# Kernel tuning notes

Hardware: AMD Instinct MI355X
Metric: run time of the kernel (lower is better)

The kernel has to match this reference:

```python
import jax, jax.numpy as jnp
import numpy as np

B, S, D, H = 4, 2048, 1024, 16
HD = D // H  # head_dim = 64

def setup_inputs() -> dict:
    key = jax.random.key(0)
    ks = jax.random.split(key, 5)
    scale = 1.0 / np.sqrt(D)
    return {
        "x": jax.random.normal(ks[0], (B, S, D), dtype=jnp.float32),
        "Wqkv": jax.random.normal(ks[1], (D, 3 * D), dtype=jnp.float32) * scale,
        "bqkv": jax.random.normal(ks[2], (3 * D,), dtype=jnp.float32) * 0.01,
        "Wo": jax.random.normal(ks[3], (D, D), dtype=jnp.float32) * scale,
        "bo": jax.random.normal(ks[4], (D,), dtype=jnp.float32) * 0.01,
    }

def reference(x, Wqkv, bqkv, Wo, bo):
    b, s, d = x.shape
    # fused QKV projection: [B,S,3D]
    qkv = jnp.einsum("bsd,de->bse", x, Wqkv) + bqkv
    # [B,S,H,3*HD] -> [B,H,S,3*HD], then chunk into q,k,v per head
    qkv = qkv.reshape(b, s, H, 3 * HD).transpose(0, 2, 1, 3)
    q, k, v = jnp.split(qkv, 3, axis=-1)  # each [B,H,S,HD]
    inv_sqrt_dk = jnp.asarray(1.0 / np.sqrt(HD), dtype=x.dtype)
    scores = jnp.einsum("bhqd,bhkd->bhqk", q, k) * inv_sqrt_dk
    attn = jax.nn.softmax(scores, axis=-1)
    values = jnp.einsum("bhqk,bhkd->bhqd", attn, v)  # [B,H,S,HD]
    # NOTE: source reshapes [B,H,S,HD] -> [B,S,H*HD] WITHOUT permuting back
    # (a quirk of the original code); replicated faithfully.
    values = values.reshape(b, s, d)
    out = jnp.einsum("bsd,de->bse", values, Wo) + bo
    return out
```

## Files before the change

kernel.cpp:

```cpp
#include <hip/hip_runtime.h>
#include <hip/hip_bf16.h>
#include <cstdint>

static constexpr int Bq  = 4;
static constexpr int Sq  = 2048;
static constexpr int Dq  = 1024;
static constexpr int Hq  = 16;
static constexpr int HDq = 64;
static constexpr int ROWS = Bq * Sq;
static constexpr int QKV_N = 3 * Dq;

typedef __bf16 bf16x8 __attribute__((ext_vector_type(8)));
typedef __bf16 bf16x4 __attribute__((ext_vector_type(4)));
typedef __bf16 bf16x2 __attribute__((ext_vector_type(2)));
typedef float  floatx4 __attribute__((ext_vector_type(4)));
typedef float  floatx16 __attribute__((ext_vector_type(16)));
typedef unsigned int uintx4 __attribute__((ext_vector_type(4)));

#define MFMA16(a, b, c) __builtin_amdgcn_mfma_f32_16x16x32_bf16((a), (b), (c), 0, 0, 0)
#define MFMA32(a, b, c) __builtin_amdgcn_mfma_f32_32x32x16_bf16((a), (b), (c), 0, 0, 0)

#define QSCALE 0.18033688011112042f

__device__ __forceinline__ void async16(const void* g, void* l) {
    __builtin_amdgcn_global_load_lds(
        (const __attribute__((address_space(1))) uint32_t*)g,
        (__attribute__((address_space(3))) uint32_t*)l, 16, 0, 0);
}

__global__ __launch_bounds__(256) void prep_kernel(const float4* __restrict__ x4,
                                                   bf16x4* __restrict__ xb4,
                                                   const float* __restrict__ Wqkv,
                                                   __bf16* __restrict__ WqkvT,
                                                   const float* __restrict__ Wo,
                                                   __bf16* __restrict__ WoT) {
    __shared__ float t[32][33];
    const int bx = blockIdx.x;
    if (bx < 8192) {
        int i = bx * 256 + threadIdx.x;
        float4 v = x4[i];
        bf16x4 o;
        o[0] = (__bf16)v.x; o[1] = (__bf16)v.y; o[2] = (__bf16)v.z; o[3] = (__bf16)v.w;
        xb4[i] = o;
        return;
    }
    const float* in; __bf16* out; int K, N, bid;
    if (bx < 8192 + 3072) { bid = bx - 8192;  in = Wqkv; out = WqkvT; K = Dq; N = QKV_N; }
    else                  { bid = bx - 11264; in = Wo;   out = WoT;   K = Dq; N = Dq; }
    const int nt = N / 32;
    const int n0 = (bid % nt) * 32, k0 = (bid / nt) * 32;
    const int c = threadIdx.x & 31, r0 = threadIdx.x >> 5;
#pragma unroll
    for (int rr = 0; rr < 32; rr += 8)
        t[r0 + rr][c] = in[(size_t)(k0 + r0 + rr) * N + n0 + c];
    __syncthreads();
#pragma unroll
    for (int rr = 0; rr < 32; rr += 8)
        out[(size_t)(n0 + r0 + rr) * K + k0 + c] = (__bf16)t[c][r0 + rr];
}

__global__ __launch_bounds__(512, 2) void gemm_qkv_kernel(const __bf16* __restrict__ A,
                                                          const __bf16* __restrict__ BT,
                                                          const float* __restrict__ bias,
                                                          __bf16* __restrict__ qkvb,
                                                          __bf16* __restrict__ Vt) {
    __shared__ __bf16 lds[2][2][2][128][64];

    const int tid  = threadIdx.x;
    const int lane = tid & 63;
    const int wave = tid >> 6;
    const int wm = wave >> 2;
    const int wn = wave & 3;
    const int l31 = lane & 31;
    const int hi  = lane >> 5;
    const int kx  = l31 & 7;

    const int m0 = blockIdx.y * 256;
    const int n0 = blockIdx.x * 256;

    const int srow = lane >> 3;
    const int ssl  = ((lane & 7) ^ srow) * 8;
    const __bf16* gA = A  + (size_t)(m0 + wave * 16 + srow) * 1024 + ssl;
    const __bf16* gB = BT + (size_t)(n0 + wave * 16 + srow) * 1024 + ssl;

    auto STAGE = [&](int buf, int op, int half, int ktel) {
        const __bf16* g = (op ? gB : gA) + (size_t)half * (128 * 1024) + ktel;
        __bf16* l = &lds[buf][op][half][0][0] + wave * 1024 + lane * 8;
        async16(g, l);
        async16(g + 8 * 1024, l + 512);
    };

    floatx16 acc[4][2] = {};

    STAGE(0, 1, 0, 0);
    STAGE(0, 0, 0, 0);
    STAGE(0, 1, 1, 0);
    STAGE(0, 0, 1, 0);
    STAGE(1, 1, 0, 64);
    STAGE(1, 0, 0, 64);
    asm volatile("s_waitcnt vmcnt(4)" ::: "memory");
    __builtin_amdgcn_sched_barrier(0);
    __builtin_amdgcn_s_barrier();

    const int brow = (wn & 1) * 64;

    for (int t = 0; t < 16; ++t) {
        const int d = t & 1;
        const __bf16* As = &lds[d][0][wm][0][0];
        const __bf16* Bs = &lds[d][1][wn >> 1][0][0];

        bf16x8 af[2][4], bf0[4], bf1[4];

#pragma unroll
        for (int mf = 0; mf < 2; ++mf)
#pragma unroll
            for (int ks = 0; ks < 4; ++ks)
                af[mf][ks] = *(const bf16x8*)(As + (mf * 32 + l31) * 64 + ((ks * 2 + hi) ^ kx) * 8);
#pragma unroll
        for (int ks = 0; ks < 4; ++ks)
            bf0[ks] = *(const bf16x8*)(Bs + (brow + l31) * 64 + ((ks * 2 + hi) ^ kx) * 8);
        if (t + 1 < 16) STAGE(d ^ 1, 1, 1, (t + 1) * 64);
        __builtin_amdgcn_s_barrier();
        __builtin_amdgcn_s_setprio(1);
#pragma unroll
        for (int ks = 0; ks < 4; ++ks) {
            acc[0][0] = MFMA32(af[0][ks], bf0[ks], acc[0][0]);
            acc[1][0] = MFMA32(af[1][ks], bf0[ks], acc[1][0]);
        }
        __builtin_amdgcn_s_setprio(0);
        __builtin_amdgcn_s_barrier();

#pragma unroll
        for (int ks = 0; ks < 4; ++ks)
            bf1[ks] = *(const bf16x8*)(Bs + (brow + 32 + l31) * 64 + ((ks * 2 + hi) ^ kx) * 8);
        if (t + 1 < 16) STAGE(d ^ 1, 0, 1, (t + 1) * 64);
        __builtin_amdgcn_s_barrier();
        __builtin_amdgcn_s_setprio(1);
#pragma unroll
        for (int ks = 0; ks < 4; ++ks) {
            acc[0][1] = MFMA32(af[0][ks], bf1[ks], acc[0][1]);
            acc[1][1] = MFMA32(af[1][ks], bf1[ks], acc[1][1]);
        }
        __builtin_amdgcn_s_setprio(0);
        __builtin_amdgcn_s_barrier();

#pragma unroll
        for (int mf = 0; mf < 2; ++mf)
#pragma unroll
            for (int ks = 0; ks < 4; ++ks)
                af[mf][ks] = *(const bf16x8*)(As + ((2 + mf) * 32 + l31) * 64 + ((ks * 2 + hi) ^ kx) * 8);
        if (t + 2 < 16) STAGE(d, 1, 0, (t + 2) * 64);
        __builtin_amdgcn_s_barrier();
        __builtin_amdgcn_s_setprio(1);
#pragma unroll
        for (int ks = 0; ks < 4; ++ks) {
            acc[2][1] = MFMA32(af[0][ks], bf1[ks], acc[2][1]);
            acc[3][1] = MFMA32(af[1][ks], bf1[ks], acc[3][1]);
        }
        __builtin_amdgcn_s_setprio(0);
        __builtin_amdgcn_s_barrier();

        if (t + 2 < 16) STAGE(d, 0, 0, (t + 2) * 64);
        __builtin_amdgcn_s_barrier();
        __builtin_amdgcn_s_setprio(1);
#pragma unroll
        for (int ks = 0; ks < 4; ++ks) {
            acc[2][0] = MFMA32(af[0][ks], bf0[ks], acc[2][0]);
            acc[3][0] = MFMA32(af[1][ks], bf0[ks], acc[3][0]);
        }
        __builtin_amdgcn_s_setprio(0);
        if (t < 14) {
            asm volatile("s_waitcnt vmcnt(4)" ::: "memory");
        } else {
            asm volatile("s_waitcnt vmcnt(0)" ::: "memory");
        }
        __builtin_amdgcn_sched_barrier(0);
        __builtin_amdgcn_s_barrier();
    }

#pragma unroll
    for (int fn = 0; fn < 2; ++fn) {
        const int cg = n0 + wn * 64 + fn * 32;
        const int cm = cg % 192;
        const float bv = bias[cg + l31];
        if (cm >= 128) {
            const int hh = cg / 192;
            const int dd = cm - 128 + l31;
            const int bb = m0 >> 11;
            const int sb = (m0 + wm * 128) & 2047;
            __bf16* vt = Vt + ((size_t)(bb * Hq + hh) * HDq + dd) * Sq + sb;
#pragma unroll
            for (int fm = 0; fm < 4; ++fm)
#pragma unroll
                for (int g = 0; g < 4; ++g) {
                    bf16x4 vv;
#pragma unroll
                    for (int i = 0; i < 4; ++i) vv[i] = (__bf16)(acc[fm][fn][g * 4 + i] + bv);
                    *(bf16x4*)(vt + fm * 32 + g * 8 + hi * 4) = vv;
                }
        } else {
            const float sc = (cm < 64) ? QSCALE : 1.0f;
#pragma unroll
            for (int fm = 0; fm < 4; ++fm)
#pragma unroll
                for (int r = 0; r < 16; ++r) {
                    int m = m0 + wm * 128 + fm * 32 + (r & 3) + 8 * (r >> 2) + 4 * hi;
                    qkvb[(size_t)m * QKV_N + cg + l31] = (__bf16)((acc[fm][fn][r] + bv) * sc);
                }
        }
    }
}

__global__ __launch_bounds__(256) void gemm_out_kernel(const __bf16* __restrict__ A,
                                                       const __bf16* __restrict__ BT,
                                                       const float* __restrict__ bias,
                                                       float* __restrict__ Cout,
                                                       int M, int N, int K) {
    __shared__ __bf16 As[128 * 32];
    __shared__ __bf16 Bs[128 * 32];

    const int t = threadIdx.x;
    const int lane = t & 63;
    const int wave = t >> 6;
    const int wm = wave & 1, wn = wave >> 1;
    const int l15 = lane & 15;
    const int kg = (lane >> 4) * 8;

    const int m0 = blockIdx.y * 128;
    const int n0 = blockIdx.x * 128;

    const int srow = t >> 2;
    const int scol = (t & 3) * 8;
    const __bf16* ag = A  + (size_t)(m0 + srow) * K + scol;
    const __bf16* bg = BT + (size_t)(n0 + srow) * K + scol;
    __bf16* al = As + t * 8;
    __bf16* bl = Bs + t * 8;

    floatx4 acc[4][4] = {};

    for (int k0 = 0; k0 < K; k0 += 32) {
        __syncthreads();
        async16(ag + k0,                    al);
        async16(ag + (size_t)64 * K + k0,   al + 2048);
        async16(bg + k0,                    bl);
        async16(bg + (size_t)64 * K + k0,   bl + 2048);
        __syncthreads();

        bf16x8 af[4], bfr[4];
#pragma unroll
        for (int mi = 0; mi < 4; ++mi)
            af[mi] = *(const bf16x8*)(As + (wm * 64 + mi * 16 + l15) * 32 + kg);
#pragma unroll
        for (int ni = 0; ni < 4; ++ni)
            bfr[ni] = *(const bf16x8*)(Bs + (wn * 64 + ni * 16 + l15) * 32 + kg);
#pragma unroll
        for (int mi = 0; mi < 4; ++mi)
#pragma unroll
            for (int ni = 0; ni < 4; ++ni)
                acc[mi][ni] = MFMA16(af[mi], bfr[ni], acc[mi][ni]);
    }

    const int r0 = (lane >> 4) * 4;
    const int wn0 = n0 + wn * 64;

#pragma unroll
    for (int ni = 0; ni < 4; ++ni) {
        int col = wn0 + ni * 16 + l15;
        float bv = bias[col];
#pragma unroll
        for (int mi = 0; mi < 4; ++mi) {
#pragma unroll
            for (int i = 0; i < 4; ++i) {
                int row = m0 + wm * 64 + mi * 16 + r0 + i;
                Cout[(size_t)row * N + col] = acc[mi][ni][i] + bv;
            }
        }
    }
}

__global__ __launch_bounds__(256, 2) void attn_kernel(const __bf16* __restrict__ qkv,
                                                      const __bf16* __restrict__ Vt,
                                                      __bf16* __restrict__ v2) {
    const int bh = blockIdx.x;
    const int b = bh >> 4, h = bh & 15;
    const int q0 = blockIdx.y * 256;
    const int tid  = threadIdx.x;
    const int lane = tid & 63;
    const int wave = tid >> 6;
    const int l31  = lane & 31;
    const int hi   = lane >> 5;
    const int kx   = l31 & 7;
    const size_t rs = QKV_N;
    const __bf16* base  = qkv + (size_t)b * Sq * rs + (size_t)h * (3 * HDq);
    const __bf16* vbase = Vt + (size_t)bh * HDq * Sq;

    __shared__ alignas(16) __bf16 Ks[2][64][64];
    __shared__ alignas(16) __bf16 Vs[2][64][64];

    bf16x8 qb[2][4];
#pragma unroll
    for (int qg = 0; qg < 2; ++qg) {
        const __bf16* qr = base + (size_t)(q0 + wave * 64 + qg * 32 + l31) * rs + hi * 8;
#pragma unroll
        for (int st = 0; st < 4; ++st) qb[qg][st] = *(const bf16x8*)(qr + st * 16);
    }

    const int rA = wave * 8 + (lane >> 3);
    const int rB = rA + 32;
    const int sw = ((lane & 7) ^ (rA & 7)) * 8;
    const __bf16* gK0 = base + HDq + (size_t)rA * rs + sw;
    const __bf16* gK1 = base + HDq + (size_t)rB * rs + sw;
    const __bf16* gV0 = vbase + (size_t)rA * Sq + sw;
    const __bf16* gV1 = vbase + (size_t)rB * Sq + sw;
    const int loff0 = wave * 512 + lane * 8;
    const int loff1 = (4 + wave) * 512 + lane * 8;

    auto STAGE = [&](int bufi, int kt) {
        const size_t ko = (size_t)kt * rs;
        async16(gK0 + ko, &Ks[bufi][0][0] + loff0);
        async16(gK1 + ko, &Ks[bufi][0][0] + loff1);
        async16(gV0 + kt, &Vs[bufi][0][0] + loff0);
        async16(gV1 + kt, &Vs[bufi][0][0] + loff1);
    };

    auto softmax_pb = [&](const floatx16& c, float& la, bf16x8* pb) {
        unsigned int W[8];
        float s0 = 0.f, s1 = 0.f;
#pragma unroll
        for (int m = 0; m < 8; ++m) {
            float e0 = __builtin_amdgcn_exp2f(c[2 * m]);
            float e1 = __builtin_amdgcn_exp2f(c[2 * m + 1]);
            s0 += e0; s1 += e1;
            union { bf16x2 v; unsigned int u; } pk;
            pk.v[0] = (__bf16)e0; pk.v[1] = (__bf16)e1;
            W[m] = pk.u;
        }
        la += s0 + s1;
#pragma unroll
        for (int ks = 0; ks < 2; ++ks) {
            auto r0 = __builtin_amdgcn_permlane32_swap(W[ks * 4 + 0], W[ks * 4 + 2], false, false);
            auto r1 = __builtin_amdgcn_permlane32_swap(W[ks * 4 + 1], W[ks * 4 + 3], false, false);
            uintx4 bb; bb[0] = r0[0]; bb[1] = r1[0]; bb[2] = r0[1]; bb[3] = r1[1];
            pb[ks] = __builtin_bit_cast(bf16x8, bb);
        }
    };

    floatx16 o[2][2] = {};
    float la0 = 0.f, la1 = 0.f;

    STAGE(0, 0);
    __syncthreads();

    int cur = 0;
    for (int kt = 0; kt < Sq; kt += 64, cur ^= 1) {
        if (kt + 64 < Sq) STAGE(cur ^ 1, kt + 64);

        bf16x8 ka0[4], ka1[4];
#pragma unroll
        for (int st = 0; st < 4; ++st) {
            ka0[st] = *(const bf16x8*)(&Ks[cur][l31][((st * 2 + hi) ^ kx) * 8]);
            ka1[st] = *(const bf16x8*)(&Ks[cur][32 + l31][((st * 2 + hi) ^ kx) * 8]);
        }
        floatx16 c00 = {}, c01 = {}, c10 = {}, c11 = {};
        __builtin_amdgcn_s_setprio(1);
#pragma unroll
        for (int st = 0; st < 4; ++st) {
            c00 = MFMA32(ka0[st], qb[0][st], c00);
            c10 = MFMA32(ka1[st], qb[0][st], c10);
            c01 = MFMA32(ka0[st], qb[1][st], c01);
            c11 = MFMA32(ka1[st], qb[1][st], c11);
        }
        __builtin_amdgcn_s_setprio(0);

        bf16x8 pb00[2], pb01[2], pb10[2], pb11[2];
        softmax_pb(c00, la0, pb00);
        softmax_pb(c01, la1, pb01);
        __builtin_amdgcn_s_setprio(1);
#pragma unroll
        for (int ks = 0; ks < 2; ++ks) {
            const int kslot = ks * 2 + hi;
            bf16x8 va0 = *(const bf16x8*)(&Vs[cur][l31][(kslot ^ kx) * 8]);
            bf16x8 va1 = *(const bf16x8*)(&Vs[cur][32 + l31][(kslot ^ kx) * 8]);
            o[0][0] = MFMA32(va0, pb00[ks], o[0][0]);
            o[0][1] = MFMA32(va1, pb00[ks], o[0][1]);
            o[1][0] = MFMA32(va0, pb01[ks], o[1][0]);
            o[1][1] = MFMA32(va1, pb01[ks], o[1][1]);
        }
        __builtin_amdgcn_s_setprio(0);
        softmax_pb(c10, la0, pb10);
        softmax_pb(c11, la1, pb11);
        __builtin_amdgcn_s_setprio(1);
#pragma unroll
        for (int ks = 0; ks < 2; ++ks) {
            const int kslot = 4 + ks * 2 + hi;
            bf16x8 va0 = *(const bf16x8*)(&Vs[cur][l31][(kslot ^ kx) * 8]);
            bf16x8 va1 = *(const bf16x8*)(&Vs[cur][32 + l31][(kslot ^ kx) * 8]);
            o[0][0] = MFMA32(va0, pb10[ks], o[0][0]);
            o[0][1] = MFMA32(va1, pb10[ks], o[0][1]);
            o[1][0] = MFMA32(va0, pb11[ks], o[1][0]);
            o[1][1] = MFMA32(va1, pb11[ks], o[1][1]);
        }
        __builtin_amdgcn_s_setprio(0);

        __syncthreads();
    }

#pragma unroll
    for (int qg = 0; qg < 2; ++qg) {
        float lsum = qg ? la1 : la0;
        float l = lsum + __shfl_xor(lsum, 32);
        float rinv = 1.0f / l;
        const int q = q0 + wave * 64 + qg * 32 + l31;
        size_t row = (size_t)b * Sq + h * 128 + (q >> 4);
        __bf16* vrow = v2 + row * Dq + (size_t)(q & 15) * 64;
#pragma unroll
        for (int gg = 0; gg < 4; ++gg) {
            bf16x4 ov;
#pragma unroll
            for (int i = 0; i < 4; ++i) ov[i] = (__bf16)(o[qg][0][gg * 4 + i] * rinv);
            *(bf16x4*)(vrow + gg * 8 + hi * 4) = ov;
#pragma unroll
            for (int i = 0; i < 4; ++i) ov[i] = (__bf16)(o[qg][1][gg * 4 + i] * rinv);
            *(bf16x4*)(vrow + 32 + gg * 8 + hi * 4) = ov;
        }
    }
}

extern "C" void kernel_launch(void* const* d_in, const int* in_sizes, int n_in,
                              void* d_out, int out_size, void* d_ws, size_t ws_size,
                              hipStream_t stream) {
    const float* x    = (const float*)d_in[0];
    const float* Wqkv = (const float*)d_in[1];
    const float* bqkv = (const float*)d_in[2];
    const float* Wo   = (const float*)d_in[3];
    const float* bo   = (const float*)d_in[4];
    float* out = (float*)d_out;

    __bf16* xb    = (__bf16*)d_ws;
    __bf16* WqkvT = xb    + (size_t)ROWS * Dq;
    __bf16* WoT   = WqkvT + (size_t)QKV_N * Dq;
    __bf16* qkvb  = WoT   + (size_t)Dq * Dq;
    __bf16* Vt    = qkvb  + (size_t)ROWS * QKV_N;
    __bf16* v2    = xb;

    prep_kernel<<<12288, 256, 0, stream>>>((const float4*)x, (bf16x4*)xb,
                                           Wqkv, WqkvT, Wo, WoT);

    gemm_qkv_kernel<<<dim3(QKV_N / 256, ROWS / 256), 512, 0, stream>>>(
        xb, WqkvT, bqkv, qkvb, Vt);

    attn_kernel<<<dim3(Bq * Hq, Sq / 256), 256, 0, stream>>>(qkvb, Vt, v2);

    gemm_out_kernel<<<dim3(Dq / 128, ROWS / 128), 256, 0, stream>>>(
        v2, WoT, bo, out, ROWS, Dq, Dq);
}
```

Before: 269.6 us.

## Retile QKV GEMM to 256x192 head-aligned blocks with 4x2 wave layout

```diff
diff --git a/kernel.cpp b/kernel.cpp
--- a/kernel.cpp
+++ b/kernel.cpp
@@ -64,109 +64,110 @@
                                                           const float* __restrict__ bias,
                                                           __bf16* __restrict__ qkvb,
                                                           __bf16* __restrict__ Vt) {
-    __shared__ __bf16 lds[2][2][2][128][64];
+    __shared__ __bf16 lds[2][7][64][64];
 
     const int tid  = threadIdx.x;
     const int lane = tid & 63;
     const int wave = tid >> 6;
-    const int wm = wave >> 2;
-    const int wn = wave & 3;
+    const int wm = wave >> 1;
+    const int wn = wave & 1;
     const int l31 = lane & 31;
     const int hi  = lane >> 5;
     const int kx  = l31 & 7;
 
     const int m0 = blockIdx.y * 256;
-    const int n0 = blockIdx.x * 256;
-
-    const int srow = lane >> 3;
-    const int ssl  = ((lane & 7) ^ srow) * 8;
-    const __bf16* gA = A  + (size_t)(m0 + wave * 16 + srow) * 1024 + ssl;
-    const __bf16* gB = BT + (size_t)(n0 + wave * 16 + srow) * 1024 + ssl;
-
-    auto STAGE = [&](int buf, int op, int half, int ktel) {
-        const __bf16* g = (op ? gB : gA) + (size_t)half * (128 * 1024) + ktel;
-        __bf16* l = &lds[buf][op][half][0][0] + wave * 1024 + lane * 8;
-        async16(g, l);
-        async16(g + 8 * 1024, l + 512);
+    const int n0 = blockIdx.x * 192;
+
+    const int sw = ((lane & 7) ^ (lane >> 3)) * 8;
+    const __bf16* gA = A  + (size_t)(m0 + wave * 8 + (lane >> 3)) * 1024 + sw;
+    const __bf16* gB = BT + (size_t)(n0 + wave * 8 + (lane >> 3)) * 1024 + sw;
+
+    auto STAGEA = [&](int buf, int u, int ktel) {
+        async16(gA + (size_t)u * 65536 + ktel, &lds[buf][u][0][0] + wave * 512 + lane * 8);
     };
-
-    floatx16 acc[4][2] = {};
-
-    STAGE(0, 1, 0, 0);
-    STAGE(0, 0, 0, 0);
-    STAGE(0, 1, 1, 0);
-    STAGE(0, 0, 1, 0);
-    STAGE(1, 1, 0, 64);
-    STAGE(1, 0, 0, 64);
+    auto STAGEB = [&](int buf, int j, int ktel) {
+        async16(gB + (size_t)j * 65536 + ktel, &lds[buf][4 + j][0][0] + wave * 512 + lane * 8);
+    };
+
+    floatx16 acc[2][3] = {};
+
+#pragma unroll
+    for (int u = 0; u < 4; ++u) STAGEA(0, u, 0);
+#pragma unroll
+    for (int j = 0; j < 3; ++j) STAGEB(0, j, 0);
+#pragma unroll
+    for (int u = 0; u < 4; ++u) STAGEA(1, u, 64);
     asm volatile("s_waitcnt vmcnt(4)" ::: "memory");
     __builtin_amdgcn_sched_barrier(0);
     __builtin_amdgcn_s_barrier();
 
-    const int brow = (wn & 1) * 64;
+    bf16x8 af[2][4], bf[4];
 
     for (int t = 0; t < 16; ++t) {
         const int d = t & 1;
-        const __bf16* As = &lds[d][0][wm][0][0];
-        const __bf16* Bs = &lds[d][1][wn >> 1][0][0];
-
-        bf16x8 af[2][4], bf0[4], bf1[4];
-
-#pragma unroll
-        for (int mf = 0; mf < 2; ++mf)
+
+#pragma unroll
+        for (int fm = 0; fm < 2; ++fm)
 #pragma unroll
             for (int ks = 0; ks < 4; ++ks)
-                af[mf][ks] = *(const bf16x8*)(As + (mf * 32 + l31) * 64 + ((ks * 2 + hi) ^ kx) * 8);
-#pragma unroll
-        for (int ks = 0; ks < 4; ++ks)
-            bf0[ks] = *(const bf16x8*)(Bs + (brow + l31) * 64 + ((ks * 2 + hi) ^ kx) * 8);
-        if (t + 1 < 16) STAGE(d ^ 1, 1, 1, (t + 1) * 64);
+                af[fm][ks] = *(const bf16x8*)(&lds[d][wm][fm * 32 + l31][((ks * 2 + hi) ^ kx) * 8]);
+        {
+            const int br = wn * 96;
+#pragma unroll
+            for (int ks = 0; ks < 4; ++ks)
+                bf[ks] = *(const bf16x8*)(&lds[d][4 + (br >> 6)][(br & 63) + l31][((ks * 2 + hi) ^ kx) * 8]);
+        }
+        if (t + 1 < 16) {
+            STAGEB(d ^ 1, 0, (t + 1) * 64);
+            STAGEB(d ^ 1, 1, (t + 1) * 64);
+            STAGEB(d ^ 1, 2, (t + 1) * 64);
+        }
         __builtin_amdgcn_s_barrier();
         __builtin_amdgcn_s_setprio(1);
 #pragma unroll
         for (int ks = 0; ks < 4; ++ks) {
-            acc[0][0] = MFMA32(af[0][ks], bf0[ks], acc[0][0]);
-            acc[1][0] = MFMA32(af[1][ks], bf0[ks], acc[1][0]);
-        }
-        __builtin_amdgcn_s_setprio(0);
-        __builtin_amdgcn_s_barrier();
-
-#pragma unroll
-        for (int ks = 0; ks < 4; ++ks)
-            bf1[ks] = *(const bf16x8*)(Bs + (brow + 32 + l31) * 64 + ((ks * 2 + hi) ^ kx) * 8);
-        if (t + 1 < 16) STAGE(d ^ 1, 0, 1, (t + 1) * 64);
+            acc[0][0] = MFMA32(af[0][ks], bf[ks], acc[0][0]);
+            acc[1][0] = MFMA32(af[1][ks], bf[ks], acc[1][0]);
+        }
+        __builtin_amdgcn_s_setprio(0);
+        __builtin_amdgcn_s_barrier();
+
+        {
+            const int br = wn * 96 + 32;
+#pragma unroll
+            for (int ks = 0; ks < 4; ++ks)
+                bf[ks] = *(const bf16x8*)(&lds[d][4 + (br >> 6)][(br & 63) + l31][((ks * 2 + hi) ^ kx) * 8]);
+        }
+        if (t + 2 < 16) {
+            STAGEA(d, 0, (t + 2) * 64);
+            STAGEA(d, 1, (t + 2) * 64);
+        }
         __builtin_amdgcn_s_barrier();
         __builtin_amdgcn_s_setprio(1);
 #pragma unroll
         for (int ks = 0; ks < 4; ++ks) {
-            acc[0][1] = MFMA32(af[0][ks], bf1[ks], acc[0][1]);
-            acc[1][1] = MFMA32(af[1][ks], bf1[ks], acc[1][1]);
-        }
-        __builtin_amdgcn_s_setprio(0);
-        __builtin_amdgcn_s_barrier();
-
-#pragma unroll
-        for (int mf = 0; mf < 2; ++mf)
+            acc[0][1] = MFMA32(af[0][ks], bf[ks], acc[0][1]);
+            acc[1][1] = MFMA32(af[1][ks], bf[ks], acc[1][1]);
+        }
+        __builtin_amdgcn_s_setprio(0);
+        __builtin_amdgcn_s_barrier();
+
+        {
+            const int br = wn * 96 + 64;
 #pragma unroll
             for (int ks = 0; ks < 4; ++ks)
-                af[mf][ks] = *(const bf16x8*)(As + ((2 + mf) * 32 + l31) * 64 + ((ks * 2 + hi) ^ kx) * 8);
-        if (t + 2 < 16) STAGE(d, 1, 0, (t + 2) * 64);
+                bf[ks] = *(const bf16x8*)(&lds[d][4 + (br >> 6)][(br & 63) + l31][((ks * 2 + hi) ^ kx) * 8]);
+        }
+        if (t + 2 < 16) {
+            STAGEA(d, 2, (t + 2) * 64);
+            STAGEA(d, 3, (t + 2) * 64);
+        }
         __builtin_amdgcn_s_barrier();
         __builtin_amdgcn_s_setprio(1);
 #pragma unroll
         for (int ks = 0; ks < 4; ++ks) {
-            acc[2][1] = MFMA32(af[0][ks], bf1[ks], acc[2][1]);
-            acc[3][1] = MFMA32(af[1][ks], bf1[ks], acc[3][1]);
-        }
-        __builtin_amdgcn_s_setprio(0);
-        __builtin_amdgcn_s_barrier();
-
-        if (t + 2 < 16) STAGE(d, 0, 0, (t + 2) * 64);
-        __builtin_amdgcn_s_barrier();
-        __builtin_amdgcn_s_setprio(1);
-#pragma unroll
-        for (int ks = 0; ks < 4; ++ks) {
-            acc[2][0] = MFMA32(af[0][ks], bf0[ks], acc[2][0]);
-            acc[3][0] = MFMA32(af[1][ks], bf0[ks], acc[3][0]);
+            acc[0][2] = MFMA32(af[0][ks], bf[ks], acc[0][2]);
+            acc[1][2] = MFMA32(af[1][ks], bf[ks], acc[1][2]);
         }
         __builtin_amdgcn_s_setprio(0);
         if (t < 14) {
@@ -179,18 +180,18 @@
     }
 
 #pragma unroll
-    for (int fn = 0; fn < 2; ++fn) {
-        const int cg = n0 + wn * 64 + fn * 32;
-        const int cm = cg % 192;
+    for (int fn = 0; fn < 3; ++fn) {
+        const int cm = wn * 96 + fn * 32;
+        const int cg = n0 + cm;
         const float bv = bias[cg + l31];
         if (cm >= 128) {
-            const int hh = cg / 192;
+            const int hh = n0 / 192;
             const int dd = cm - 128 + l31;
             const int bb = m0 >> 11;
-            const int sb = (m0 + wm * 128) & 2047;
+            const int sb = (m0 & 2047) + wm * 64;
             __bf16* vt = Vt + ((size_t)(bb * Hq + hh) * HDq + dd) * Sq + sb;
 #pragma unroll
-            for (int fm = 0; fm < 4; ++fm)
+            for (int fm = 0; fm < 2; ++fm)
 #pragma unroll
                 for (int g = 0; g < 4; ++g) {
                     bf16x4 vv;
@@ -201,10 +202,10 @@
         } else {
             const float sc = (cm < 64) ? QSCALE : 1.0f;
 #pragma unroll
-            for (int fm = 0; fm < 4; ++fm)
+            for (int fm = 0; fm < 2; ++fm)
 #pragma unroll
                 for (int r = 0; r < 16; ++r) {
-                    int m = m0 + wm * 128 + fm * 32 + (r & 3) + 8 * (r >> 2) + 4 * hi;
+                    int m = m0 + wm * 64 + fm * 32 + (r & 3) + 8 * (r >> 2) + 4 * hi;
                     qkvb[(size_t)m * QKV_N + cg + l31] = (__bf16)((acc[fm][fn][r] + bv) * sc);
                 }
         }
@@ -446,7 +447,7 @@
     prep_kernel<<<12288, 256, 0, stream>>>((const float4*)x, (bf16x4*)xb,
                                            Wqkv, WqkvT, Wo, WoT);
 
-    gemm_qkv_kernel<<<dim3(QKV_N / 256, ROWS / 256), 512, 0, stream>>>(
+    gemm_qkv_kernel<<<dim3(QKV_N / 192, ROWS / 256), 512, 0, stream>>>(
         xb, WqkvT, bqkv, qkvb, Vt);
 
     attn_kernel<<<dim3(Bq * Hq, Sq / 256), 256, 0, stream>>>(qkvb, Vt, v2);
```

New measurement: 267.5 us. Within noise of the previous version (-0.8%).
